# Optimization experiments

Measured on AMD Instinct MI355X. Metric: run time of the kernel, lower is better.

## Reference

```python
import jax, jax.numpy as jnp
import numpy as np

H, DK, OUT, IN = 8, 64, 512, 512
N, E = 30000, 100000
SQRT_DK = float(np.sqrt(DK))


def _lin_params(k, din, dout):
    kw, = jax.random.split(k, 1)
    w = jax.random.normal(kw, (din, dout), jnp.float32) * (1.0 / np.sqrt(din))
    b = jnp.zeros((dout,), jnp.float32)
    return w, b


def setup_inputs() -> dict:
    key = jax.random.key(0)
    ks = jax.random.split(key, 24)
    inp = {
        'h_paper': jax.random.normal(ks[0], (N, IN), jnp.float32),
        'h_author': jax.random.normal(ks[1], (N, IN), jnp.float32),
        'src0': jax.random.randint(ks[2], (E,), 0, N),  # author ids
        'dst0': jax.random.randint(ks[3], (E,), 0, N),  # paper ids
        'src1': jax.random.randint(ks[4], (E,), 0, N),  # paper ids
        'dst1': jax.random.randint(ks[5], (E,), 0, N),  # author ids
    }
    # per-node-type linears (type 0 = paper, type 1 = author)
    i = 6
    for t in (0, 1):
        for nm in ('Wk', 'Wq', 'Wv', 'Wa'):
            w, b = _lin_params(ks[i], IN, OUT)
            inp[f'{nm}{t}'] = w
            inp[f'b{nm[1].lower()}{t}'] = b
            i += 1
    # relation parameters (xavier ~ uniform scaled; normal approx is fine for a reference)
    inp['rel_att'] = jax.random.normal(ks[22], (2, H, DK, DK), jnp.float32) * (1.0 / np.sqrt(DK))
    inp['rel_msg'] = jax.random.normal(ks[23], (2, H, DK, DK), jnp.float32) * (1.0 / np.sqrt(DK))
    inp['rel_pri'] = jnp.ones((2, H), jnp.float32)
    inp['skip'] = jnp.ones((2,), jnp.float32)
    return inp


def _relation_agg(h_src, Wk, bk, Wv, bv, h_dst, Wq, bq, src, dst, A, M, pri):
    # project src/dst node features to multi-head k/v/q: [N, H, DK]
    k = (h_src @ Wk + bk).reshape(-1, H, DK)
    v = (h_src @ Wv + bv).reshape(-1, H, DK)
    q = (h_dst @ Wq + bq).reshape(-1, H, DK)
    # per-edge relation-specific transforms (HGT Step 1/2)
    key_e = jnp.einsum('ehk,hkd->ehd', k[src], A)   # [E,H,DK]
    val_e = jnp.einsum('ehk,hkd->ehd', v[src], M)   # [E,H,DK]
    att = (q[dst] * key_e).sum(-1) * pri / SQRT_DK  # [E,H]
    # segment softmax over incoming edges of each destination node
    m = jax.ops.segment_max(att, dst, num_segments=N)
    m = jnp.where(jnp.isfinite(m), m, 0.0)
    e = jnp.exp(att - m[dst])
    s = jax.ops.segment_sum(e, dst, num_segments=N)
    a = e / s[dst]                                   # [E,H]
    t = jax.ops.segment_sum(a[..., None] * val_e, dst, num_segments=N)
    return t.reshape(N, OUT)


def reference(h_paper, h_author, src0, dst0, src1, dst1,
              Wk0, bk0, Wq0, bq0, Wv0, bv0, Wa0, ba0,
              Wk1, bk1, Wq1, bq1, Wv1, bv1, Wa1, ba1,
              rel_att, rel_msg, rel_pri, skip):
    # relation 0: author (type 1) -> paper (type 0)
    t_paper = _relation_agg(h_author, Wk1, bk1, Wv1, bv1, h_paper, Wq0, bq0,
                            src0, dst0, rel_att[0], rel_msg[0], rel_pri[0])
    # relation 1: paper (type 0) -> author (type 1)
    t_author = _relation_agg(h_paper, Wk0, bk0, Wv0, bv0, h_author, Wq1, bq1,
                             src1, dst1, rel_att[1], rel_msg[1], rel_pri[1])
    # Step 3: target-specific aggregation with sigmoid skip (dropout=0 -> identity)
    a0 = jax.nn.sigmoid(skip[0])
    a1 = jax.nn.sigmoid(skip[1])
    out_paper = (t_paper @ Wa0 + ba0) * a0 + h_paper * (1.0 - a0)
    out_author = (t_author @ Wa1 + ba1) * a1 + h_author * (1.0 - a1)
    return jnp.stack([out_paper, out_author])  # [2, N, OUT]
```

## Files before the change

kernel.cpp:

```cpp
#include <hip/hip_runtime.h>
#include <hip/hip_bf16.h>
#include <stdint.h>

#define N_NODES 30000
#define N_PAD   30080
#define N_EDGES 100000
#define DIM     512
#define QKV_LD  1536

typedef unsigned short ushort_t;
typedef __attribute__((ext_vector_type(8))) short short8;
typedef __attribute__((ext_vector_type(8))) unsigned short ushortx8;
typedef __attribute__((ext_vector_type(4))) float floatx4;

__device__ __forceinline__ float b2f(ushort_t b) { return __uint_as_float(((unsigned)b) << 16); }
__device__ __forceinline__ ushort_t f2b(float f) {
    unsigned u = __float_as_uint(f);
    u += 0x7FFFu + ((u >> 16) & 1u);
    return (ushort_t)(u >> 16);
}

__global__ __launch_bounds__(256) void pad_copy2(const float* __restrict__ h0,
                                                 const float* __restrict__ h1,
                                                 ushort_t* __restrict__ d0,
                                                 ushort_t* __restrict__ d1) {
    const int total = N_PAD * DIM / 4;
    const int valid = N_NODES * DIM / 4;
    int idx = blockIdx.x * 256 + threadIdx.x;
    if (idx >= total) return;
    const float* s = blockIdx.y ? h1 : h0;
    ushort_t* d = blockIdx.y ? d1 : d0;
    float4 v = make_float4(0.f, 0.f, 0.f, 0.f);
    if (idx < valid) v = ((const float4*)s)[idx];
    ushort_t o[4] = {f2b(v.x), f2b(v.y), f2b(v.z), f2b(v.w)};
    ((uint2*)d)[idx] = *(const uint2*)o;
}

__global__ __launch_bounds__(256) void fuse_weights4(const float* __restrict__ Wk0, const float* __restrict__ bk0,
                                                     const float* __restrict__ Wv0, const float* __restrict__ bv0,
                                                     const float* __restrict__ Wk1, const float* __restrict__ bk1,
                                                     const float* __restrict__ Wv1, const float* __restrict__ bv1,
                                                     const float* __restrict__ rel_att, const float* __restrict__ rel_msg,
                                                     ushort_t* __restrict__ cat_p, ushort_t* __restrict__ cat_a,
                                                     float* __restrict__ bias_p, float* __restrict__ bias_a) {
    const float *W, *bvec, *A;
    ushort_t* outw; float* outb;
    switch (blockIdx.y) {
        case 0: W = Wk1; bvec = bk1; A = rel_att;          outw = cat_a + 512 * DIM;  outb = bias_a + 512;  break;
        case 1: W = Wv1; bvec = bv1; A = rel_msg;          outw = cat_a + 1024 * DIM; outb = bias_a + 1024; break;
        case 2: W = Wk0; bvec = bk0; A = rel_att + 32768;  outw = cat_p + 512 * DIM;  outb = bias_p + 512;  break;
        default: W = Wv0; bvec = bv0; A = rel_msg + 32768; outw = cat_p + 1024 * DIM; outb = bias_p + 1024; break;
    }
    int idx = blockIdx.x * 256 + threadIdx.x;
    int n = idx & 511;
    int i = idx >> 9;
    int h = n >> 6, d = n & 63;
    const float* wrow = W + i * DIM + h * 64;
    const float* acol = A + h * 4096 + d;
    float s = 0.f;
#pragma unroll 8
    for (int c = 0; c < 64; ++c) s += wrow[c] * acol[c * 64];
    outw[n * DIM + i] = f2b(s);
    if (i == 0) {
        const float* bh = bvec + h * 64;
        float sb = 0.f;
        for (int c = 0; c < 64; ++c) sb += bh[c] * acol[c * 64];
        outb[n] = sb;
    }
}

__global__ __launch_bounds__(256) void transpose4(const float* w0, const float* w1,
                                                  const float* w2, const float* w3,
                                                  ushort_t* o0, ushort_t* o1,
                                                  ushort_t* o2, ushort_t* o3) {
    const float* W; ushort_t* O;
    switch (blockIdx.y) {
        case 0: W = w0; O = o0; break;
        case 1: W = w1; O = o1; break;
        case 2: W = w2; O = o2; break;
        default: W = w3; O = o3; break;
    }
    __shared__ float tile[32][33];
    int bx = blockIdx.x & 15, by = blockIdx.x >> 4;
    int tx = threadIdx.x & 31, ty = threadIdx.x >> 5;
#pragma unroll
    for (int r = 0; r < 32; r += 8) tile[ty + r][tx] = W[(by * 32 + ty + r) * DIM + bx * 32 + tx];
    __syncthreads();
#pragma unroll
    for (int r = 0; r < 32; r += 8) O[(bx * 32 + ty + r) * DIM + by * 32 + tx] = f2b(tile[tx][ty + r]);
}

__global__ __launch_bounds__(256) void copy_biases(const float* bq0, const float* bq1,
                                                   float* bias_p, float* bias_a) {
    int i = blockIdx.x * 256 + threadIdx.x;
    bias_p[i] = bq0[i];
    bias_a[i] = bq1[i];
}

__global__ __launch_bounds__(256) void hist2(const int* __restrict__ dst0, const int* __restrict__ dst1,
                                             int* __restrict__ cnt) {
    int e = blockIdx.x * 256 + threadIdx.x;
    if (e >= 2 * N_EDGES) return;
    int rel = e >= N_EDGES;
    int d = (rel ? dst1 : dst0)[e - rel * N_EDGES];
    atomicAdd(&cnt[rel * N_NODES + d], 1);
}

__global__ __launch_bounds__(1024) void scan2(const int* __restrict__ cnt, int* __restrict__ row_ptr) {
    int rel = blockIdx.x;
    const int* c = cnt + rel * N_NODES;
    int* rp = row_ptr + rel * (N_NODES + 1);
    __shared__ int sums[1024];
    int tid = threadIdx.x;
    int base = tid * 32;
    int loc[32];
    int s = 0;
#pragma unroll
    for (int i = 0; i < 32; ++i) {
        int idx = base + i;
        int v = (idx < N_NODES) ? c[idx] : 0;
        s += v;
        loc[i] = s;
    }
    sums[tid] = s;
    __syncthreads();
    for (int off = 1; off < 1024; off <<= 1) {
        int add = (tid >= off) ? sums[tid - off] : 0;
        __syncthreads();
        sums[tid] += add;
        __syncthreads();
    }
    int pre = (tid > 0) ? sums[tid - 1] : 0;
    if (tid == 0) rp[0] = 0;
#pragma unroll
    for (int i = 0; i < 32; ++i) {
        int idx = base + i;
        if (idx < N_NODES) rp[idx + 1] = pre + loc[i];
    }
}

__global__ __launch_bounds__(256) void scatter2(const int* __restrict__ src0, const int* __restrict__ dst0,
                                                const int* __restrict__ src1, const int* __restrict__ dst1,
                                                const int* __restrict__ row_ptr,
                                                int* __restrict__ fill,
                                                int* __restrict__ colarr) {
    int e = blockIdx.x * 256 + threadIdx.x;
    if (e >= 2 * N_EDGES) return;
    int rel = e >= N_EDGES;
    int ei = e - rel * N_EDGES;
    int s = (rel ? src1 : src0)[ei];
    int d = (rel ? dst1 : dst0)[ei];
    int pos = atomicAdd(&fill[rel * N_NODES + d], 1);
    colarr[rel * N_EDGES + row_ptr[rel * (N_NODES + 1) + d] + pos] = s;
}

typedef const __attribute__((address_space(1))) unsigned int gu32;
typedef __attribute__((address_space(3))) unsigned int lu32;
__device__ __forceinline__ void gload_lds16(const void* g, void* l) {
    __builtin_amdgcn_global_load_lds((gu32*)g, (lu32*)l, 16, 0, 0);
}

__global__ __launch_bounds__(512) void gemm_proj(const ushort_t* __restrict__ Ap, const ushort_t* __restrict__ Aa,
                                                 const ushort_t* __restrict__ Bp, const ushort_t* __restrict__ Ba,
                                                 const float* __restrict__ bias_p, const float* __restrict__ bias_a,
                                                 ushort_t* __restrict__ Cp, ushort_t* __restrict__ Ca) {
    int bid = blockIdx.x;
    int lin = (bid & 7) * 705 + (bid >> 3);
    int rel = lin >= 2820;
    int r = lin - rel * 2820;
    int my = r / 12, nx = r - my * 12;
    const ushort_t* A = rel ? Aa : Ap;
    const ushort_t* BT = rel ? Ba : Bp;
    const float* bias = rel ? bias_a : bias_p;
    ushort_t* C = rel ? Ca : Cp;

    __shared__ alignas(16) ushort_t As[128 * 32];
    __shared__ alignas(16) ushort_t Bs[128 * 32];
    int n0 = nx * 128, m0 = my * 128;
    int tid = threadIdx.x;
    int w = tid >> 6, l = tid & 63;
    int wr = w >> 1, wc = w & 1;
    int fr = l & 15, fq = l >> 4;
    floatx4 acc[2][4] = {};
    int aXor = (fr >> 1) & 3;
    const ushort_t* aF = &As[(wr * 32 + fr) * 32 + (fq ^ aXor) * 8];
    const ushort_t* bF = &Bs[(wc * 64 + fr) * 32 + (fq ^ aXor) * 8];
    int g = tid & 255;
    int srow = g >> 2;
    int sc0 = (((g & 3) ^ ((srow >> 1) & 3))) * 8;
    const ushort_t* gsrc0 = (tid < 256) ? (A + (size_t)(m0 + srow) * DIM + sc0)
                                        : (BT + (size_t)(n0 + srow) * DIM + sc0);
    const ushort_t* gsrc1 = gsrc0 + (size_t)64 * DIM;
    char* ldst = (tid < 256) ? ((char*)As + g * 16) : ((char*)Bs + g * 16);

#pragma unroll 1
    for (int kt = 0; kt < 16; ++kt) {
        int k0 = kt * 32;
        if (kt) __syncthreads();
        gload_lds16(gsrc0 + k0, ldst);
        gload_lds16(gsrc1 + k0, ldst + 4096);
        __syncthreads();
        short8 af[2], bf[4];
#pragma unroll
        for (int i = 0; i < 2; ++i) af[i] = *(const short8*)(aF + i * 16 * 32);
#pragma unroll
        for (int j = 0; j < 4; ++j) bf[j] = *(const short8*)(bF + j * 16 * 32);
#pragma unroll
        for (int i = 0; i < 2; ++i)
#pragma unroll
            for (int j = 0; j < 4; ++j)
                acc[i][j] = __builtin_amdgcn_mfma_f32_16x16x32_bf16(af[i], bf[j], acc[i][j], 0, 0, 0);
    }
#pragma unroll
    for (int i = 0; i < 2; ++i)
#pragma unroll
        for (int j = 0; j < 4; ++j) {
            int col = n0 + wc * 64 + j * 16 + fr;
            float bc = bias[col];
#pragma unroll
            for (int rr = 0; rr < 4; ++rr) {
                int grow = m0 + wr * 32 + i * 16 + fq * 4 + rr;
                C[(size_t)grow * QKV_LD + col] = f2b(acc[i][j][rr] + bc);
            }
        }
}

__global__ __launch_bounds__(512) void gemm_out(const ushort_t* __restrict__ Tp, const ushort_t* __restrict__ Ta,
                                                const ushort_t* __restrict__ Wp, const ushort_t* __restrict__ Wa,
                                                const float* __restrict__ ba0, const float* __restrict__ ba1,
                                                const ushort_t* __restrict__ hp, const ushort_t* __restrict__ ha,
                                                const float* __restrict__ skipv, float* __restrict__ out) {
    int bid = blockIdx.x;
    int lin = (bid & 7) * 235 + (bid >> 3);
    int rel = lin >= 940;
    int r = lin - rel * 940;
    int my = r >> 2, nx = r & 3;
    const ushort_t* A = rel ? Ta : Tp;
    const ushort_t* BT = rel ? Wa : Wp;
    const float* bias = rel ? ba1 : ba0;
    const ushort_t* Hres = rel ? ha : hp;
    float* C = out + (size_t)rel * N_NODES * DIM;

    __shared__ alignas(16) ushort_t As[128 * 32];
    __shared__ alignas(16) ushort_t Bs[128 * 32];
    int n0 = nx * 128, m0 = my * 128;
    int tid = threadIdx.x;
    int w = tid >> 6, l = tid & 63;
    int wr = w >> 1, wc = w & 1;
    int fr = l & 15, fq = l >> 4;
    floatx4 acc[2][4] = {};
    int aXor = (fr >> 1) & 3;
    const ushort_t* aF = &As[(wr * 32 + fr) * 32 + (fq ^ aXor) * 8];
    const ushort_t* bF = &Bs[(wc * 64 + fr) * 32 + (fq ^ aXor) * 8];
    int g = tid & 255;
    int srow = g >> 2;
    int sc0 = (((g & 3) ^ ((srow >> 1) & 3))) * 8;
    const ushort_t* gsrc0 = (tid < 256) ? (A + (size_t)(m0 + srow) * QKV_LD + sc0)
                                        : (BT + (size_t)(n0 + srow) * DIM + sc0);
    const ushort_t* gsrc1 = gsrc0 + (size_t)64 * ((tid < 256) ? QKV_LD : DIM);
    char* ldst = (tid < 256) ? ((char*)As + g * 16) : ((char*)Bs + g * 16);

#pragma unroll 1
    for (int kt = 0; kt < 16; ++kt) {
        int k0 = kt * 32;
        if (kt) __syncthreads();
        gload_lds16(gsrc0 + k0, ldst);
        gload_lds16(gsrc1 + k0, ldst + 4096);
        __syncthreads();
        short8 af[2], bf[4];
#pragma unroll
        for (int i = 0; i < 2; ++i) af[i] = *(const short8*)(aF + i * 16 * 32);
#pragma unroll
        for (int j = 0; j < 4; ++j) bf[j] = *(const short8*)(bF + j * 16 * 32);
#pragma unroll
        for (int i = 0; i < 2; ++i)
#pragma unroll
            for (int j = 0; j < 4; ++j)
                acc[i][j] = __builtin_amdgcn_mfma_f32_16x16x32_bf16(af[i], bf[j], acc[i][j], 0, 0, 0);
    }
    float sk = skipv[rel];
    float alpha = 1.f / (1.f + __expf(-sk));
    float onem = 1.f - alpha;
#pragma unroll
    for (int i = 0; i < 2; ++i)
#pragma unroll
        for (int j = 0; j < 4; ++j) {
            int col = n0 + wc * 64 + j * 16 + fr;
            float bc = bias[col];
#pragma unroll
            for (int rr = 0; rr < 4; ++rr) {
                int grow = m0 + wr * 32 + i * 16 + fq * 4 + rr;
                if (grow < N_NODES) {
                    float v = acc[i][j][rr] + bc;
                    float hres = b2f(Hres[(size_t)grow * DIM + col]);
                    C[(size_t)grow * DIM + col] = v * alpha + hres * onem;
                }
            }
        }
}

__global__ __launch_bounds__(256) void node_attn(const ushort_t* __restrict__ qkv_p,
                                                 ushort_t* __restrict__ qkv_p_mut,
                                                 const ushort_t* __restrict__ qkv_a,
                                                 ushort_t* __restrict__ qkv_a_mut,
                                                 const int* __restrict__ row_ptr,
                                                 const int* __restrict__ colarr,
                                                 const float* __restrict__ rel_pri) {
    int rel = blockIdx.y;
    const ushort_t* qkv_dst = rel ? qkv_a : qkv_p;
    ushort_t* t_out = rel ? qkv_a_mut : qkv_p_mut;
    const ushort_t* qkv_src = rel ? qkv_p : qkv_a;
    const int* rp = row_ptr + rel * (N_NODES + 1);
    const int* col = colarr + rel * N_EDGES;
    const float* pri = rel_pri + rel * 8;

    int w = threadIdx.x >> 6, l = threadIdx.x & 63;
    int n = blockIdx.x * 4 + w;
    float prih = pri[l >> 3] * 0.125f;

    size_t qoff = (size_t)n * QKV_LD + l * 8;
    ushortx8 qr = *(const ushortx8*)(qkv_dst + qoff);
    float qd[8];
#pragma unroll
    for (int i = 0; i < 8; ++i) qd[i] = b2f(qr[i]);

    int lo = 0, hi = 0;
    if (n < N_NODES) { lo = rp[n]; hi = rp[n + 1]; }

    float m = -3.0e38f, s = 0.f;
    float acc[8] = {};
    int j = lo;
    ushortx8 kr, vr;
    if (j < hi) {
        int sn = col[j];
        const ushort_t* kb = qkv_src + (size_t)sn * QKV_LD + 512 + l * 8;
        kr = *(const ushortx8*)kb;
        vr = *(const ushortx8*)(kb + 512);
    }
    while (j < hi) {
        ushortx8 kc = kr, vc = vr;
        ++j;
        if (j < hi) {
            int sn = col[j];
            const ushort_t* kb = qkv_src + (size_t)sn * QKV_LD + 512 + l * 8;
            kr = *(const ushortx8*)kb;
            vr = *(const ushortx8*)(kb + 512);
        }
        float dot = 0.f;
#pragma unroll
        for (int i = 0; i < 8; ++i) dot += qd[i] * b2f(kc[i]);
        dot += __shfl_xor(dot, 1);
        dot += __shfl_xor(dot, 2);
        dot += __shfl_xor(dot, 4);
        float att = dot * prih;
        float mn = fmaxf(m, att);
        float e0 = __expf(m - mn);
        float e1 = __expf(att - mn);
        s = s * e0 + e1;
#pragma unroll
        for (int i = 0; i < 8; ++i) acc[i] = acc[i] * e0 + e1 * b2f(vc[i]);
        m = mn;
    }
    float inv = (hi > lo) ? 1.f / s : 0.f;
    ushortx8 o;
#pragma unroll
    for (int i = 0; i < 8; ++i) o[i] = f2b(acc[i] * inv);
    *(ushortx8*)(t_out + qoff) = o;
}

extern "C" void kernel_launch(void* const* d_in, const int* in_sizes, int n_in,
                              void* d_out, int out_size, void* d_ws, size_t ws_size,
                              hipStream_t stream) {
    (void)in_sizes; (void)n_in; (void)out_size; (void)ws_size;
    const float* h_paper  = (const float*)d_in[0];
    const float* h_author = (const float*)d_in[1];
    const int* src0 = (const int*)d_in[2];
    const int* dst0 = (const int*)d_in[3];
    const int* src1 = (const int*)d_in[4];
    const int* dst1 = (const int*)d_in[5];
    const float* Wk0 = (const float*)d_in[6];  const float* bk0 = (const float*)d_in[7];
    const float* Wq0 = (const float*)d_in[8];  const float* bq0 = (const float*)d_in[9];
    const float* Wv0 = (const float*)d_in[10]; const float* bv0 = (const float*)d_in[11];
    const float* Wa0 = (const float*)d_in[12]; const float* ba0 = (const float*)d_in[13];
    const float* Wk1 = (const float*)d_in[14]; const float* bk1 = (const float*)d_in[15];
    const float* Wq1 = (const float*)d_in[16]; const float* bq1 = (const float*)d_in[17];
    const float* Wv1 = (const float*)d_in[18]; const float* bv1 = (const float*)d_in[19];
    const float* Wa1 = (const float*)d_in[20]; const float* ba1 = (const float*)d_in[21];
    const float* rel_att = (const float*)d_in[22];
    const float* rel_msg = (const float*)d_in[23];
    const float* rel_pri = (const float*)d_in[24];
    const float* skipv   = (const float*)d_in[25];
    float* out = (float*)d_out;

    char* p = (char*)d_ws;
    auto alloc = [&](size_t bytes) -> char* {
        char* r = p;
        p += (bytes + 255) & ~(size_t)255;
        return r;
    };
    ushort_t* hp_pad = (ushort_t*)alloc((size_t)N_PAD * DIM * 2);
    ushort_t* ha_pad = (ushort_t*)alloc((size_t)N_PAD * DIM * 2);
    ushort_t* qkv_p = (ushort_t*)alloc((size_t)N_PAD * QKV_LD * 2);
    ushort_t* qkv_a = (ushort_t*)alloc((size_t)N_PAD * QKV_LD * 2);
    ushort_t* cat_p = (ushort_t*)alloc((size_t)QKV_LD * DIM * 2);
    ushort_t* cat_a = (ushort_t*)alloc((size_t)QKV_LD * DIM * 2);
    ushort_t* WaT0 = (ushort_t*)alloc(DIM * DIM * 2);
    ushort_t* WaT1 = (ushort_t*)alloc(DIM * DIM * 2);
    float* bias_p = (float*)alloc(QKV_LD * 4);
    float* bias_a = (float*)alloc(QKV_LD * 4);
    int* cnt = (int*)alloc((size_t)4 * N_NODES * 4);
    int* fill = cnt + 2 * N_NODES;
    int* row_ptr = (int*)alloc((size_t)2 * (N_NODES + 1) * 4);
    int* colarr = (int*)alloc((size_t)2 * N_EDGES * 4);

    pad_copy2<<<dim3((N_PAD * DIM / 4 + 255) / 256, 2), 256, 0, stream>>>(h_paper, h_author, hp_pad, ha_pad);
    fuse_weights4<<<dim3(1024, 4), 256, 0, stream>>>(Wk0, bk0, Wv0, bv0, Wk1, bk1, Wv1, bv1,
                                                     rel_att, rel_msg, cat_p, cat_a, bias_p, bias_a);
    transpose4<<<dim3(256, 4), 256, 0, stream>>>(Wq0, Wq1, Wa0, Wa1, cat_p, cat_a, WaT0, WaT1);
    copy_biases<<<2, 256, 0, stream>>>(bq0, bq1, bias_p, bias_a);

    hipMemsetAsync(cnt, 0, (size_t)4 * N_NODES * 4, stream);
    hist2<<<(2 * N_EDGES + 255) / 256, 256, 0, stream>>>(dst0, dst1, cnt);
    scan2<<<2, 1024, 0, stream>>>(cnt, row_ptr);
    scatter2<<<(2 * N_EDGES + 255) / 256, 256, 0, stream>>>(src0, dst0, src1, dst1, row_ptr, fill, colarr);

    gemm_proj<<<5640, 512, 0, stream>>>(hp_pad, ha_pad, cat_p, cat_a, bias_p, bias_a, qkv_p, qkv_a);

    node_attn<<<dim3(N_PAD / 4, 2), 256, 0, stream>>>(qkv_p, qkv_p, qkv_a, qkv_a, row_ptr, colarr, rel_pri);

    gemm_out<<<1880, 512, 0, stream>>>(qkv_p, qkv_a, WaT0, WaT1, ba0, ba1,
                                       hp_pad, ha_pad, skipv, out);
}
```

Baseline: 644.3 us.

## Double GEMM K-tile to 64 and split edge softmax into two accumulators

Both projection and output GEMMs now stage a 64-wide K slice per iteration with a new XOR swizzle, halving the number of barrier-separated iterations and issuing more MFMAs per sync. The edge aggregation kernel replaces its one-ahead prefetch loop with a two-edge unrolled loop that keeps two independent online-softmax states and merges them at the end. This exposes more memory-level parallelism on gathered K/V rows, at the cost of more registers and double the LDS per block.

Result: no change. 637.3 us (-1.1%).

```diff
diff --git a/kernel.cpp b/kernel.cpp
--- a/kernel.cpp
+++ b/kernel.cpp
@@ -174,42 +174,52 @@
     const float* bias = rel ? bias_a : bias_p;
     ushort_t* C = rel ? Ca : Cp;
 
-    __shared__ alignas(16) ushort_t As[128 * 32];
-    __shared__ alignas(16) ushort_t Bs[128 * 32];
+    __shared__ alignas(16) ushort_t As[128 * 64];
+    __shared__ alignas(16) ushort_t Bs[128 * 64];
     int n0 = nx * 128, m0 = my * 128;
     int tid = threadIdx.x;
     int w = tid >> 6, l = tid & 63;
     int wr = w >> 1, wc = w & 1;
     int fr = l & 15, fq = l >> 4;
     floatx4 acc[2][4] = {};
-    int aXor = (fr >> 1) & 3;
-    const ushort_t* aF = &As[(wr * 32 + fr) * 32 + (fq ^ aXor) * 8];
-    const ushort_t* bF = &Bs[(wc * 64 + fr) * 32 + (fq ^ aXor) * 8];
-    int g = tid & 255;
-    int srow = g >> 2;
-    int sc0 = (((g & 3) ^ ((srow >> 1) & 3))) * 8;
-    const ushort_t* gsrc0 = (tid < 256) ? (A + (size_t)(m0 + srow) * DIM + sc0)
-                                        : (BT + (size_t)(n0 + srow) * DIM + sc0);
-    const ushort_t* gsrc1 = gsrc0 + (size_t)64 * DIM;
-    char* ldst = (tid < 256) ? ((char*)As + g * 16) : ((char*)Bs + g * 16);
+    int s0 = fq ^ (fr & 7);
+    const ushort_t* aF0 = &As[(wr * 32 + fr) * 64 + s0 * 8];
+    const ushort_t* aF1 = &As[(wr * 32 + fr) * 64 + (s0 ^ 4) * 8];
+    const ushort_t* bF0 = &Bs[(wc * 64 + fr) * 64 + s0 * 8];
+    const ushort_t* bF1 = &Bs[(wc * 64 + fr) * 64 + (s0 ^ 4) * 8];
+    int tq = tid & 255;
+    int r0 = tq >> 3;
+    int ss = ((tq & 7) ^ (r0 & 7)) * 8;
+    const ushort_t* gsrc = (tid < 256) ? (A + (size_t)(m0 + r0) * DIM + ss)
+                                       : (BT + (size_t)(n0 + r0) * DIM + ss);
+    char* ldst = (tid < 256) ? ((char*)As + tq * 16) : ((char*)Bs + tq * 16);
 
 #pragma unroll 1
-    for (int kt = 0; kt < 16; ++kt) {
-        int k0 = kt * 32;
+    for (int kt = 0; kt < 8; ++kt) {
+        int k0 = kt * 64;
         if (kt) __syncthreads();
-        gload_lds16(gsrc0 + k0, ldst);
-        gload_lds16(gsrc1 + k0, ldst + 4096);
+#pragma unroll
+        for (int q = 0; q < 4; ++q)
+            gload_lds16(gsrc + k0 + (size_t)q * 32 * DIM, ldst + q * 4096);
         __syncthreads();
-        short8 af[2], bf[4];
-#pragma unroll
-        for (int i = 0; i < 2; ++i) af[i] = *(const short8*)(aF + i * 16 * 32);
-#pragma unroll
-        for (int j = 0; j < 4; ++j) bf[j] = *(const short8*)(bF + j * 16 * 32);
-#pragma unroll
-        for (int i = 0; i < 2; ++i)
-#pragma unroll
-            for (int j = 0; j < 4; ++j)
-                acc[i][j] = __builtin_amdgcn_mfma_f32_16x16x32_bf16(af[i], bf[j], acc[i][j], 0, 0, 0);
+        short8 af[2][2], bf[2][4];
+#pragma unroll
+        for (int i = 0; i < 2; ++i) {
+            af[0][i] = *(const short8*)(aF0 + i * 16 * 64);
+            af[1][i] = *(const short8*)(aF1 + i * 16 * 64);
+        }
+#pragma unroll
+        for (int j = 0; j < 4; ++j) {
+            bf[0][j] = *(const short8*)(bF0 + j * 16 * 64);
+            bf[1][j] = *(const short8*)(bF1 + j * 16 * 64);
+        }
+#pragma unroll
+        for (int kk = 0; kk < 2; ++kk)
+#pragma unroll
+            for (int i = 0; i < 2; ++i)
+#pragma unroll
+                for (int j = 0; j < 4; ++j)
+                    acc[i][j] = __builtin_amdgcn_mfma_f32_16x16x32_bf16(af[kk][i], bf[kk][j], acc[i][j], 0, 0, 0);
     }
 #pragma unroll
     for (int i = 0; i < 2; ++i)
@@ -241,42 +251,53 @@
     const ushort_t* Hres = rel ? ha : hp;
     float* C = out + (size_t)rel * N_NODES * DIM;
 
-    __shared__ alignas(16) ushort_t As[128 * 32];
-    __shared__ alignas(16) ushort_t Bs[128 * 32];
+    __shared__ alignas(16) ushort_t As[128 * 64];
+    __shared__ alignas(16) ushort_t Bs[128 * 64];
     int n0 = nx * 128, m0 = my * 128;
     int tid = threadIdx.x;
     int w = tid >> 6, l = tid & 63;
     int wr = w >> 1, wc = w & 1;
     int fr = l & 15, fq = l >> 4;
     floatx4 acc[2][4] = {};
-    int aXor = (fr >> 1) & 3;
-    const ushort_t* aF = &As[(wr * 32 + fr) * 32 + (fq ^ aXor) * 8];
-    const ushort_t* bF = &Bs[(wc * 64 + fr) * 32 + (fq ^ aXor) * 8];
-    int g = tid & 255;
-    int srow = g >> 2;
-    int sc0 = (((g & 3) ^ ((srow >> 1) & 3))) * 8;
-    const ushort_t* gsrc0 = (tid < 256) ? (A + (size_t)(m0 + srow) * QKV_LD + sc0)
-                                        : (BT + (size_t)(n0 + srow) * DIM + sc0);
-    const ushort_t* gsrc1 = gsrc0 + (size_t)64 * ((tid < 256) ? QKV_LD : DIM);
-    char* ldst = (tid < 256) ? ((char*)As + g * 16) : ((char*)Bs + g * 16);
+    int s0 = fq ^ (fr & 7);
+    const ushort_t* aF0 = &As[(wr * 32 + fr) * 64 + s0 * 8];
+    const ushort_t* aF1 = &As[(wr * 32 + fr) * 64 + (s0 ^ 4) * 8];
+    const ushort_t* bF0 = &Bs[(wc * 64 + fr) * 64 + s0 * 8];
+    const ushort_t* bF1 = &Bs[(wc * 64 + fr) * 64 + (s0 ^ 4) * 8];
+    int tq = tid & 255;
+    int r0 = tq >> 3;
+    int ss = ((tq & 7) ^ (r0 & 7)) * 8;
+    size_t lda = (tid < 256) ? (size_t)QKV_LD : (size_t)DIM;
+    const ushort_t* gsrc = (tid < 256) ? (A + (size_t)(m0 + r0) * QKV_LD + ss)
+                                       : (BT + (size_t)(n0 + r0) * DIM + ss);
+    char* ldst = (tid < 256) ? ((char*)As + tq * 16) : ((char*)Bs + tq * 16);
 
 #pragma unroll 1
-    for (int kt = 0; kt < 16; ++kt) {
-        int k0 = kt * 32;
+    for (int kt = 0; kt < 8; ++kt) {
+        int k0 = kt * 64;
         if (kt) __syncthreads();
-        gload_lds16(gsrc0 + k0, ldst);
-        gload_lds16(gsrc1 + k0, ldst + 4096);
+#pragma unroll
+        for (int q = 0; q < 4; ++q)
+            gload_lds16(gsrc + k0 + (size_t)q * 32 * lda, ldst + q * 4096);
         __syncthreads();
-        short8 af[2], bf[4];
-#pragma unroll
-        for (int i = 0; i < 2; ++i) af[i] = *(const short8*)(aF + i * 16 * 32);
-#pragma unroll
-        for (int j = 0; j < 4; ++j) bf[j] = *(const short8*)(bF + j * 16 * 32);
-#pragma unroll
-        for (int i = 0; i < 2; ++i)
-#pragma unroll
-            for (int j = 0; j < 4; ++j)
-                acc[i][j] = __builtin_amdgcn_mfma_f32_16x16x32_bf16(af[i], bf[j], acc[i][j], 0, 0, 0);
+        short8 af[2][2], bf[2][4];
+#pragma unroll
+        for (int i = 0; i < 2; ++i) {
+            af[0][i] = *(const short8*)(aF0 + i * 16 * 64);
+            af[1][i] = *(const short8*)(aF1 + i * 16 * 64);
+        }
+#pragma unroll
+        for (int j = 0; j < 4; ++j) {
+            bf[0][j] = *(const short8*)(bF0 + j * 16 * 64);
+            bf[1][j] = *(const short8*)(bF1 + j * 16 * 64);
+        }
+#pragma unroll
+        for (int kk = 0; kk < 2; ++kk)
+#pragma unroll
+            for (int i = 0; i < 2; ++i)
+#pragma unroll
+                for (int j = 0; j < 4; ++j)
+                    acc[i][j] = __builtin_amdgcn_mfma_f32_16x16x32_bf16(af[kk][i], bf[kk][j], acc[i][j], 0, 0, 0);
     }
     float sk = skipv[rel];
     float alpha = 1.f / (1.f + __expf(-sk));
@@ -327,44 +348,65 @@
     int lo = 0, hi = 0;
     if (n < N_NODES) { lo = rp[n]; hi = rp[n + 1]; }
 
-    float m = -3.0e38f, s = 0.f;
-    float acc[8] = {};
+    float m0v = -3.0e38f, s0v = 0.f;
+    float m1v = -3.0e38f, s1v = 0.f;
+    float acc0[8] = {}, acc1[8] = {};
     int j = lo;
-    ushortx8 kr, vr;
+    while (j + 1 < hi) {
+        int sn0 = col[j], sn1 = col[j + 1];
+        const ushort_t* kb0 = qkv_src + (size_t)sn0 * QKV_LD + 512 + l * 8;
+        const ushort_t* kb1 = qkv_src + (size_t)sn1 * QKV_LD + 512 + l * 8;
+        ushortx8 kc0 = *(const ushortx8*)kb0;
+        ushortx8 vc0 = *(const ushortx8*)(kb0 + 512);
+        ushortx8 kc1 = *(const ushortx8*)kb1;
+        ushortx8 vc1 = *(const ushortx8*)(kb1 + 512);
+        float d0 = 0.f, d1 = 0.f;
+#pragma unroll
+        for (int i = 0; i < 8; ++i) { d0 += qd[i] * b2f(kc0[i]); d1 += qd[i] * b2f(kc1[i]); }
+        d0 += __shfl_xor(d0, 1); d1 += __shfl_xor(d1, 1);
+        d0 += __shfl_xor(d0, 2); d1 += __shfl_xor(d1, 2);
+        d0 += __shfl_xor(d0, 4); d1 += __shfl_xor(d1, 4);
+        float a0 = d0 * prih, a1 = d1 * prih;
+        float mn0 = fmaxf(m0v, a0);
+        float e00 = __expf(m0v - mn0), e01 = __expf(a0 - mn0);
+        float mn1 = fmaxf(m1v, a1);
+        float e10 = __expf(m1v - mn1), e11 = __expf(a1 - mn1);
+        s0v = s0v * e00 + e01;
+        s1v = s1v * e10 + e11;
+#pragma unroll
+        for (int i = 0; i < 8; ++i) {
+            acc0[i] = acc0[i] * e00 + e01 * b2f(vc0[i]);
+            acc1[i] = acc1[i] * e10 + e11 * b2f(vc1[i]);
+        }
+        m0v = mn0; m1v = mn1;
+        j += 2;
+    }
     if (j < hi) {
         int sn = col[j];
         const ushort_t* kb = qkv_src + (size_t)sn * QKV_LD + 512 + l * 8;
-        kr = *(const ushortx8*)kb;
-        vr = *(const ushortx8*)(kb + 512);
-    }
-    while (j < hi) {
-        ushortx8 kc = kr, vc = vr;
-        ++j;
-        if (j < hi) {
-            int sn = col[j];
-            const ushort_t* kb = qkv_src + (size_t)sn * QKV_LD + 512 + l * 8;
-            kr = *(const ushortx8*)kb;
-            vr = *(const ushortx8*)(kb + 512);
-        }
-        float dot = 0.f;
-#pragma unroll
-        for (int i = 0; i < 8; ++i) dot += qd[i] * b2f(kc[i]);
-        dot += __shfl_xor(dot, 1);
-        dot += __shfl_xor(dot, 2);
-        dot += __shfl_xor(dot, 4);
-        float att = dot * prih;
-        float mn = fmaxf(m, att);
-        float e0 = __expf(m - mn);
-        float e1 = __expf(att - mn);
-        s = s * e0 + e1;
-#pragma unroll
-        for (int i = 0; i < 8; ++i) acc[i] = acc[i] * e0 + e1 * b2f(vc[i]);
-        m = mn;
-    }
+        ushortx8 kc = *(const ushortx8*)kb;
+        ushortx8 vc = *(const ushortx8*)(kb + 512);
+        float d0 = 0.f;
+#pragma unroll
+        for (int i = 0; i < 8; ++i) d0 += qd[i] * b2f(kc[i]);
+        d0 += __shfl_xor(d0, 1);
+        d0 += __shfl_xor(d0, 2);
+        d0 += __shfl_xor(d0, 4);
+        float a0 = d0 * prih;
+        float mn0 = fmaxf(m0v, a0);
+        float e00 = __expf(m0v - mn0), e01 = __expf(a0 - mn0);
+        s0v = s0v * e00 + e01;
+#pragma unroll
+        for (int i = 0; i < 8; ++i) acc0[i] = acc0[i] * e00 + e01 * b2f(vc[i]);
+        m0v = mn0;
+    }
+    float mn = fmaxf(m0v, m1v);
+    float e0 = __expf(m0v - mn), e1 = __expf(m1v - mn);
+    float s = s0v * e0 + s1v * e1;
     float inv = (hi > lo) ? 1.f / s : 0.f;
     ushortx8 o;
 #pragma unroll
-    for (int i = 0; i < 8; ++i) o[i] = f2b(acc[i] * inv);
+    for (int i = 0; i < 8; ++i) o[i] = f2b((acc0[i] * e0 + acc1[i] * e1) * inv);
     *(ushortx8*)(t_out + qoff) = o;
 }
 
```

## Triple-buffer LDS tiles in projection and output GEMMs with async prefetch

Applied to the files above, without the earlier changes.

Both bf16 MFMA GEMM kernels move from a single LDS buffer with two barriers per K-step to a three-stage LDS ring. The next K-tile is prefetched with global_load_lds while the current one is consumed, using explicit vmcnt waits and one barrier per iteration. This hides global-load latency behind MFMA work and cuts synchronisation. The cost is three times the LDS footprint (48 KB per block), which can reduce occupancy. It also depends on the triple buffering to avoid a write-after-read race without a second barrier.

New measurement: 632.6 us. About the same (-1.8%).

```diff
diff --git a/kernel.cpp b/kernel.cpp
--- a/kernel.cpp
+++ b/kernel.cpp
@@ -174,8 +174,7 @@
     const float* bias = rel ? bias_a : bias_p;
     ushort_t* C = rel ? Ca : Cp;
 
-    __shared__ alignas(16) ushort_t As[128 * 32];
-    __shared__ alignas(16) ushort_t Bs[128 * 32];
+    __shared__ alignas(16) ushort_t S[3][2][128 * 32];
     int n0 = nx * 128, m0 = my * 128;
     int tid = threadIdx.x;
     int w = tid >> 6, l = tid & 63;
@@ -183,23 +182,36 @@
     int fr = l & 15, fq = l >> 4;
     floatx4 acc[2][4] = {};
     int aXor = (fr >> 1) & 3;
-    const ushort_t* aF = &As[(wr * 32 + fr) * 32 + (fq ^ aXor) * 8];
-    const ushort_t* bF = &Bs[(wc * 64 + fr) * 32 + (fq ^ aXor) * 8];
-    int g = tid & 255;
-    int srow = g >> 2;
-    int sc0 = (((g & 3) ^ ((srow >> 1) & 3))) * 8;
+    int aoff = ((wr * 32 + fr) * 32 + (fq ^ aXor) * 8) * 2;
+    int boff = 8192 + ((wc * 64 + fr) * 32 + (fq ^ aXor) * 8) * 2;
+    int tq = tid & 255;
+    int srow = tq >> 2;
+    int sc0 = (((tq & 3) ^ ((srow >> 1) & 3))) * 8;
     const ushort_t* gsrc0 = (tid < 256) ? (A + (size_t)(m0 + srow) * DIM + sc0)
                                         : (BT + (size_t)(n0 + srow) * DIM + sc0);
     const ushort_t* gsrc1 = gsrc0 + (size_t)64 * DIM;
-    char* ldst = (tid < 256) ? ((char*)As + g * 16) : ((char*)Bs + g * 16);
-
+    char* sbase = (char*)S + ((tid < 256) ? 0 : 8192) + tq * 16;
+
+    gload_lds16(gsrc0, sbase);
+    gload_lds16(gsrc1, sbase + 4096);
+
+    int cur = 0, nxt = 1;
 #pragma unroll 1
     for (int kt = 0; kt < 16; ++kt) {
-        int k0 = kt * 32;
-        if (kt) __syncthreads();
-        gload_lds16(gsrc0 + k0, ldst);
-        gload_lds16(gsrc1 + k0, ldst + 4096);
-        __syncthreads();
+        if (kt < 15) {
+            int k1 = (kt + 1) * 32;
+            char* d = sbase + nxt * 16384;
+            gload_lds16(gsrc0 + k1, d);
+            gload_lds16(gsrc1 + k1, d + 4096);
+            asm volatile("s_waitcnt vmcnt(2)" ::: "memory");
+        } else {
+            asm volatile("s_waitcnt vmcnt(0)" ::: "memory");
+        }
+        __builtin_amdgcn_sched_barrier(0);
+        __builtin_amdgcn_s_barrier();
+        __builtin_amdgcn_sched_barrier(0);
+        const ushort_t* aF = (const ushort_t*)((const char*)S + cur * 16384 + aoff);
+        const ushort_t* bF = (const ushort_t*)((const char*)S + cur * 16384 + boff);
         short8 af[2], bf[4];
 #pragma unroll
         for (int i = 0; i < 2; ++i) af[i] = *(const short8*)(aF + i * 16 * 32);
@@ -210,6 +222,7 @@
 #pragma unroll
             for (int j = 0; j < 4; ++j)
                 acc[i][j] = __builtin_amdgcn_mfma_f32_16x16x32_bf16(af[i], bf[j], acc[i][j], 0, 0, 0);
+        cur = nxt; nxt = (nxt == 2) ? 0 : nxt + 1;
     }
 #pragma unroll
     for (int i = 0; i < 2; ++i)
@@ -241,8 +254,7 @@
     const ushort_t* Hres = rel ? ha : hp;
     float* C = out + (size_t)rel * N_NODES * DIM;
 
-    __shared__ alignas(16) ushort_t As[128 * 32];
-    __shared__ alignas(16) ushort_t Bs[128 * 32];
+    __shared__ alignas(16) ushort_t S[3][2][128 * 32];
     int n0 = nx * 128, m0 = my * 128;
     int tid = threadIdx.x;
     int w = tid >> 6, l = tid & 63;
@@ -250,23 +262,37 @@
     int fr = l & 15, fq = l >> 4;
     floatx4 acc[2][4] = {};
     int aXor = (fr >> 1) & 3;
-    const ushort_t* aF = &As[(wr * 32 + fr) * 32 + (fq ^ aXor) * 8];
-    const ushort_t* bF = &Bs[(wc * 64 + fr) * 32 + (fq ^ aXor) * 8];
-    int g = tid & 255;
-    int srow = g >> 2;
-    int sc0 = (((g & 3) ^ ((srow >> 1) & 3))) * 8;
+    int aoff = ((wr * 32 + fr) * 32 + (fq ^ aXor) * 8) * 2;
+    int boff = 8192 + ((wc * 64 + fr) * 32 + (fq ^ aXor) * 8) * 2;
+    int tq = tid & 255;
+    int srow = tq >> 2;
+    int sc0 = (((tq & 3) ^ ((srow >> 1) & 3))) * 8;
+    size_t lda = (tid < 256) ? (size_t)QKV_LD : (size_t)DIM;
     const ushort_t* gsrc0 = (tid < 256) ? (A + (size_t)(m0 + srow) * QKV_LD + sc0)
                                         : (BT + (size_t)(n0 + srow) * DIM + sc0);
-    const ushort_t* gsrc1 = gsrc0 + (size_t)64 * ((tid < 256) ? QKV_LD : DIM);
-    char* ldst = (tid < 256) ? ((char*)As + g * 16) : ((char*)Bs + g * 16);
-
+    const ushort_t* gsrc1 = gsrc0 + (size_t)64 * lda;
+    char* sbase = (char*)S + ((tid < 256) ? 0 : 8192) + tq * 16;
+
+    gload_lds16(gsrc0, sbase);
+    gload_lds16(gsrc1, sbase + 4096);
+
+    int cur = 0, nxt = 1;
 #pragma unroll 1
     for (int kt = 0; kt < 16; ++kt) {
-        int k0 = kt * 32;
-        if (kt) __syncthreads();
-        gload_lds16(gsrc0 + k0, ldst);
-        gload_lds16(gsrc1 + k0, ldst + 4096);
-        __syncthreads();
+        if (kt < 15) {
+            int k1 = (kt + 1) * 32;
+            char* d = sbase + nxt * 16384;
+            gload_lds16(gsrc0 + k1, d);
+            gload_lds16(gsrc1 + k1, d + 4096);
+            asm volatile("s_waitcnt vmcnt(2)" ::: "memory");
+        } else {
+            asm volatile("s_waitcnt vmcnt(0)" ::: "memory");
+        }
+        __builtin_amdgcn_sched_barrier(0);
+        __builtin_amdgcn_s_barrier();
+        __builtin_amdgcn_sched_barrier(0);
+        const ushort_t* aF = (const ushort_t*)((const char*)S + cur * 16384 + aoff);
+        const ushort_t* bF = (const ushort_t*)((const char*)S + cur * 16384 + boff);
         short8 af[2], bf[4];
 #pragma unroll
         for (int i = 0; i < 2; ++i) af[i] = *(const short8*)(aF + i * 16 * 32);
@@ -277,6 +303,7 @@
 #pragma unroll
             for (int j = 0; j < 4; ++j)
                 acc[i][j] = __builtin_amdgcn_mfma_f32_16x16x32_bf16(af[i], bf[j], acc[i][j], 0, 0, 0);
+        cur = nxt; nxt = (nxt == 2) ? 0 : nxt + 1;
     }
     float sk = skipv[rel];
     float alpha = 1.f / (1.f + __expf(-sk));
```
